# Kernel tuning notes

Measured on AMD Instinct MI355X. Metric: run time of the kernel, lower is better.

The kernel has to match this reference:

```python
import jax, jax.numpy as jnp
import numpy as np

N, F, M, B = 100000, 256, 10, 32768
DECAY = 0.9


def setup_inputs() -> dict:
    key = jax.random.key(0)
    ks = jax.random.split(key, 16)
    s = 1.0 / np.sqrt(F)
    # forward args
    node_indices = jax.random.permutation(ks[0], N)[:B]  # unique indices
    node_features = jax.random.normal(ks[1], (B, F), jnp.float32)
    # per-node state
    hidden_states = jax.random.normal(ks[2], (N, F), jnp.float32) * 0.1
    cell_states = jax.random.normal(ks[3], (N, F), jnp.float32) * 0.1
    temporal_memory = jax.random.normal(ks[4], (N, M, F), jnp.float32) * 0.1
    memory_ptr = jax.random.randint(ks[5], (N,), 0, M)
    # LSTMCell params (gate order i, f, g, o as in torch)
    W_ih = jax.random.normal(ks[6], (4 * F, F), jnp.float32) * s
    W_hh = jax.random.normal(ks[7], (4 * F, F), jnp.float32) * s
    b_ih = jax.random.normal(ks[8], (4 * F,), jnp.float32) * s
    b_hh = jax.random.normal(ks[9], (4 * F,), jnp.float32) * s
    # attention read params
    Wq = jax.random.normal(ks[10], (F, F), jnp.float32) * s
    bq = jnp.zeros((F,), jnp.float32)
    Wk = jax.random.normal(ks[11], (F, F), jnp.float32) * s
    bk = jnp.zeros((F,), jnp.float32)
    Wv = jax.random.normal(ks[12], (F, F), jnp.float32) * s
    bv = jnp.zeros((F,), jnp.float32)
    return dict(node_indices=node_indices, node_features=node_features,
                hidden_states=hidden_states, cell_states=cell_states,
                temporal_memory=temporal_memory, memory_ptr=memory_ptr,
                W_ih=W_ih, W_hh=W_hh, b_ih=b_ih, b_hh=b_hh,
                Wq=Wq, bq=bq, Wk=Wk, bk=bk, Wv=Wv, bv=bv)


def reference(node_indices, node_features, hidden_states, cell_states,
              temporal_memory, memory_ptr, W_ih, W_hh, b_ih, b_hh,
              Wq, bq, Wk, bk, Wv, bv):
    idx = node_indices
    feat = node_features.shape[-1]
    # --- update_memory: LSTMCell on gathered per-node states ---
    h_prev = hidden_states[idx]              # (B, F)
    c_prev = cell_states[idx]                # (B, F)
    gates = node_features @ W_ih.T + b_ih + h_prev @ W_hh.T + b_hh
    i, f, g, o = jnp.split(gates, 4, axis=-1)
    c_new = jax.nn.sigmoid(f) * c_prev + jax.nn.sigmoid(i) * jnp.tanh(g)
    h_new = jax.nn.sigmoid(o) * jnp.tanh(c_new)
    # --- scatter into circular temporal memory + decay previous slot ---
    ptr = memory_ptr[idx]                    # (B,)
    tm = temporal_memory.at[idx, ptr].set(node_features)
    prev = ptr - 1                           # -1 wraps; decay only applied if ptr > 0
    old = tm[idx, prev]                      # (B, F)
    tm = tm.at[idx, prev].set(jnp.where((ptr > 0)[:, None], old * DECAY, old))
    # --- get_temporal_context: gather + tiny attention over M slots ---
    mem = tm[idx]                            # (B, M, F)
    q = h_new @ Wq.T + bq                    # (B, F)  hidden_states[idx] post-update == h_new
    k = mem @ Wk.T + bk                      # (B, M, F)
    v = mem @ Wv.T + bv                      # (B, M, F)
    scores = jnp.einsum('bf,bmf->bm', q, k) / jnp.sqrt(jnp.asarray(feat, q.dtype))
    w = jax.nn.softmax(scores, axis=-1)      # (B, M)
    context = jnp.einsum('bmf,bm->bf', v, w) # (B, F)
    return context
```

## Files before the change

kernel.cpp:

```cpp
#include <hip/hip_runtime.h>
#include <hip/hip_bf16.h>

constexpr int NB = 32768;
constexpr int NF = 256;
constexpr int NM = 10;
constexpr float DECAY = 0.9f;

using bf16x8 = __attribute__((ext_vector_type(8))) short;
using f32x4  = __attribute__((ext_vector_type(4))) float;

static __device__ __forceinline__ ushort f2bf(float x) {
    unsigned u = __float_as_uint(x);
    unsigned r = (u + 0x7fffu + ((u >> 16) & 1u)) >> 16;
    return (ushort)r;
}
static __device__ __forceinline__ float bf2f(ushort x) {
    return __uint_as_float(((unsigned)x) << 16);
}
static __device__ __forceinline__ float sigmoid_f(float x) {
    return 1.f / (1.f + __expf(-x));
}
static __device__ __forceinline__ float tanh_f(float x) {
    float e = __expf(2.f * x);
    return (e - 1.f) / (e + 1.f);
}
static __device__ __forceinline__ void gload16(const void* g, void* l) {
    __builtin_amdgcn_global_load_lds(
        (const __attribute__((address_space(1))) unsigned int*)g,
        (__attribute__((address_space(3))) unsigned int*)l, 16, 0, 0);
}
static __device__ __forceinline__ int swzb(int row, int byteInRow) {
    return (row * 512 + byteInRow) ^ ((row & 7) << 4);
}

constexpr int PB_ACAT = 16384;
constexpr int PB_WGI  = PB_ACAT + 1024;
constexpr int PB_WQKT = PB_WGI + 256;
constexpr int PB_WV   = PB_WQKT + 256;
constexpr int PB_TOT  = PB_WV + 1;

__global__ __launch_bounds__(256) void k_prep(
    const float* __restrict__ W_ih, const float* __restrict__ W_hh,
    const float* __restrict__ b_ih, const float* __restrict__ b_hh,
    const float* __restrict__ Wq, const float* __restrict__ bq,
    const float* __restrict__ Wk, const float* __restrict__ Wv,
    const float* __restrict__ nf, const float* __restrict__ hidden,
    const int* __restrict__ idx,
    ushort* __restrict__ Wg, float* __restrict__ bsum,
    ushort* __restrict__ WqkT, float* __restrict__ bqk,
    ushort* __restrict__ Wvb, ushort* __restrict__ Acat)
{
    const int blk = blockIdx.x, tid = threadIdx.x;
    if (blk < PB_ACAT) {
        int t = blk * 256 + tid;
        int row = t >> 7;
        int c4 = (t & 127) * 4;
        const float* src = (c4 < 256) ? (nf + (size_t)row * 256 + c4)
                                      : (hidden + (size_t)idx[row] * 256 + (c4 - 256));
        float4 v = *reinterpret_cast<const float4*>(src);
        ushort4 o;
        o.x = f2bf(v.x); o.y = f2bf(v.y); o.z = f2bf(v.z); o.w = f2bf(v.w);
        *reinterpret_cast<ushort4*>(Acat + (size_t)row * 512 + c4) = o;
    } else if (blk < PB_WGI) {
        int j = blk - PB_ACAT;
        for (int c = tid; c < 512; c += 256) {
            float v = (c < 256) ? W_ih[j * 256 + c] : W_hh[j * 256 + (c - 256)];
            Wg[j * 512 + c] = f2bf(v);
        }
        if (tid == 0) bsum[j] = b_ih[j] + b_hh[j];
    } else if (blk < PB_WQKT) {
        int i = blk - PB_WGI, a = tid;
        float s = 0.f;
#pragma unroll 8
        for (int j = 0; j < 256; ++j) s += Wq[j * 256 + a] * Wk[j * 256 + i];
        WqkT[i * 256 + a] = f2bf(s * 0.0625f);
    } else if (blk < PB_WV) {
        int t = (blk - PB_WQKT) * 256 + tid;
        Wvb[t] = f2bf(Wv[t]);
    } else {
        int i = tid;
        float s = 0.f;
#pragma unroll 8
        for (int j = 0; j < 256; ++j) s += bq[j] * Wk[j * 256 + i];
        bqk[i] = s * 0.0625f;
    }
}

__global__ __launch_bounds__(256) void k_gates2(
    const ushort* __restrict__ Acat, const ushort* __restrict__ Wg,
    const float* __restrict__ bsum, const int* __restrict__ idx,
    const float* __restrict__ cell, ushort* __restrict__ h_new)
{
    __shared__ ushort As[2][128 * 32];
    __shared__ ushort Bs[2][128 * 32];
    const int t = threadIdx.x;
    const int w = t >> 6, l = t & 63;
    const int wr = w >> 1, wc = w & 1;
    const int lr = l & 15, lk = l >> 4;

    const int flat = blockIdx.x;
    const int xc = flat & 7, grp = flat >> 3;
    const int by = grp & 7;
    const int bx = (grp >> 3) * 8 + xc;
    const int row0 = bx * 128;
    const int f0 = by * 32;

    f32x4 acc[4][4];
#pragma unroll
    for (int m = 0; m < 4; ++m)
#pragma unroll
        for (int g = 0; g < 4; ++g) acc[m][g] = f32x4{0.f, 0.f, 0.f, 0.f};

    const int srow = l >> 2;
    const int scol = (l & 3) * 8;
    const int u0 = w * 2, u1 = u0 + 1;
    const ushort* aS0 = Acat + (size_t)(row0 + u0 * 16 + srow) * 512 + scol;
    const ushort* aS1 = Acat + (size_t)(row0 + u1 * 16 + srow) * 512 + scol;
    const ushort* bS0 = Wg + (size_t)(w * 256 + f0 + srow) * 512 + scol;
    const ushort* bS1 = Wg + (size_t)(w * 256 + f0 + 16 + srow) * 512 + scol;
    ushort* aL0_0 = As[0] + u0 * 512; ushort* aL1_0 = As[0] + u1 * 512;
    ushort* aL0_1 = As[1] + u0 * 512; ushort* aL1_1 = As[1] + u1 * 512;
    ushort* bL0_0 = Bs[0] + (w * 32) * 32; ushort* bL1_0 = Bs[0] + (w * 32 + 16) * 32;
    ushort* bL0_1 = Bs[1] + (w * 32) * 32; ushort* bL1_1 = Bs[1] + (w * 32 + 16) * 32;

    for (int k0 = 0; k0 < 512; k0 += 64) {
        gload16(aS0 + k0,      aL0_0);
        gload16(aS1 + k0,      aL1_0);
        gload16(aS0 + k0 + 32, aL0_1);
        gload16(aS1 + k0 + 32, aL1_1);
        gload16(bS0 + k0,      bL0_0);
        gload16(bS1 + k0,      bL1_0);
        gload16(bS0 + k0 + 32, bL0_1);
        gload16(bS1 + k0 + 32, bL1_1);
        __syncthreads();
#pragma unroll
        for (int h = 0; h < 2; ++h) {
            bf16x8 af[4], bfr[4];
#pragma unroll
            for (int m = 0; m < 4; ++m)
                af[m] = *reinterpret_cast<const bf16x8*>(As[h] + (wr * 64 + m * 16 + lr) * 32 + lk * 8);
#pragma unroll
            for (int g = 0; g < 4; ++g)
                bfr[g] = *reinterpret_cast<const bf16x8*>(Bs[h] + (g * 32 + wc * 16 + lr) * 32 + lk * 8);
#pragma unroll
            for (int m = 0; m < 4; ++m)
#pragma unroll
                for (int g = 0; g < 4; ++g)
                    acc[m][g] = __builtin_amdgcn_mfma_f32_16x16x32_bf16(af[m], bfr[g], acc[m][g], 0, 0, 0);
        }
        __syncthreads();
    }

    const int f = f0 + wc * 16 + lr;
    float bs[4];
#pragma unroll
    for (int g = 0; g < 4; ++g) bs[g] = bsum[g * 256 + f];

    int nodev[4][4];
#pragma unroll
    for (int m = 0; m < 4; ++m)
#pragma unroll
        for (int r = 0; r < 4; ++r)
            nodev[m][r] = idx[row0 + wr * 64 + m * 16 + lk * 4 + r];

#pragma unroll
    for (int m = 0; m < 4; ++m) {
#pragma unroll
        for (int r = 0; r < 4; ++r) {
            float gi = acc[m][0][r] + bs[0];
            float gf = acc[m][1][r] + bs[1];
            float gg = acc[m][2][r] + bs[2];
            float go = acc[m][3][r] + bs[3];
            float cp = cell[(size_t)nodev[m][r] * 256 + f];
            float cn = sigmoid_f(gf) * cp + sigmoid_f(gi) * tanh_f(gg);
            float hn = sigmoid_f(go) * tanh_f(cn);
            int row = row0 + wr * 64 + m * 16 + lk * 4 + r;
            h_new[(size_t)row * 256 + f] = f2bf(hn);
        }
    }
}

__global__ __launch_bounds__(256) void k_attnout(
    const ushort* __restrict__ hnew, const ushort* __restrict__ WqkT,
    const float* __restrict__ bqk, const ushort* __restrict__ Wvb,
    const float* __restrict__ bv, const int* __restrict__ idx,
    const int* __restrict__ mptr, const float* __restrict__ tm,
    const float* __restrict__ nf, float* __restrict__ out)
{
    __shared__ ushort sC[16 * 256];
    char* sB = (char*)sC;
    const int t = threadIdx.x, w = t >> 6, l = t & 63;
    const int lr = l & 15, lk = l >> 4;
    const int row0 = blockIdx.x * 16;

    {
        f32x4 qa[4];
#pragma unroll
        for (int n = 0; n < 4; ++n) qa[n] = f32x4{0.f, 0.f, 0.f, 0.f};
        const ushort* ap = hnew + (size_t)(row0 + lr) * 256 + lk * 8;
        const ushort* bp[4];
#pragma unroll
        for (int n = 0; n < 4; ++n) bp[n] = WqkT + (size_t)(w * 64 + n * 16 + lr) * 256 + lk * 8;
#pragma unroll 2
        for (int k0 = 0; k0 < 256; k0 += 32) {
            bf16x8 a = *reinterpret_cast<const bf16x8*>(ap + k0);
            bf16x8 b[4];
#pragma unroll
            for (int n = 0; n < 4; ++n) b[n] = *reinterpret_cast<const bf16x8*>(bp[n] + k0);
#pragma unroll
            for (int n = 0; n < 4; ++n)
                qa[n] = __builtin_amdgcn_mfma_f32_16x16x32_bf16(a, b[n], qa[n], 0, 0, 0);
        }
#pragma unroll
        for (int n = 0; n < 4; ++n) {
            int colc = w * 64 + n * 16 + lr;
            float bbq = bqk[colc];
#pragma unroll
            for (int r = 0; r < 4; ++r) {
                int row = lk * 4 + r;
                *(ushort*)(sB + swzb(row, colc * 2)) = f2bf(qa[n][r] + bbq);
            }
        }
    }
    __syncthreads();

    {
        const int b0 = row0 + w * 4;
        int nodes[4], ptrs[4];
#pragma unroll
        for (int r = 0; r < 4; ++r) { nodes[r] = idx[b0 + r]; ptrs[r] = mptr[nodes[r]]; }

        for (int rr = 0; rr < 4; ++rr) {
            const int row = w * 4 + rr;
            const int b = b0 + rr;
            const int node = nodes[rr];
            const int ptr = ptrs[rr];
            ushort4 q4 = *(const ushort4*)(sB + swzb(row, l * 8));
            float q0 = bf2f(q4.x), q1 = bf2f(q4.y), q2 = bf2f(q4.z), q3 = bf2f(q4.w);
            const float* base = tm + (size_t)node * (NM * NF);
            const float* nfp = nf + (size_t)b * 256 + l * 4;

            float4 mem[NM];
            float sc[NM];
#pragma unroll
            for (int m = 0; m < NM; ++m) {
                float4 v = (m == ptr) ? *reinterpret_cast<const float4*>(nfp)
                                      : *reinterpret_cast<const float4*>(base + (size_t)m * 256 + l * 4);
                if (ptr > 0 && m == ptr - 1) { v.x *= DECAY; v.y *= DECAY; v.z *= DECAY; v.w *= DECAY; }
                mem[m] = v;
                sc[m] = q0 * v.x + q1 * v.y + q2 * v.z + q3 * v.w;
            }
#pragma unroll
            for (int m = 0; m < NM; ++m) {
                float s = sc[m];
#pragma unroll
                for (int d = 1; d < 64; d <<= 1) s += __shfl_xor(s, d, 64);
                sc[m] = s;
            }
            float mx = sc[0];
#pragma unroll
            for (int m = 1; m < NM; ++m) mx = fmaxf(mx, sc[m]);
            float e[NM], sum = 0.f;
#pragma unroll
            for (int m = 0; m < NM; ++m) { e[m] = __expf(sc[m] - mx); sum += e[m]; }
            float inv = 1.f / sum;
            float4 c = {0.f, 0.f, 0.f, 0.f};
#pragma unroll
            for (int m = 0; m < NM; ++m) {
                float wm = e[m] * inv;
                c.x += wm * mem[m].x; c.y += wm * mem[m].y; c.z += wm * mem[m].z; c.w += wm * mem[m].w;
            }
            ushort4 o;
            o.x = f2bf(c.x); o.y = f2bf(c.y); o.z = f2bf(c.z); o.w = f2bf(c.w);
            *(ushort4*)(sB + swzb(row, l * 8)) = o;
        }
    }
    __syncthreads();

    f32x4 acc[4];
#pragma unroll
    for (int n = 0; n < 4; ++n) acc[n] = f32x4{0.f, 0.f, 0.f, 0.f};
    const ushort* vptr[4];
#pragma unroll
    for (int n = 0; n < 4; ++n) vptr[n] = Wvb + (size_t)(w * 64 + n * 16 + lr) * 256 + lk * 8;

#pragma unroll 2
    for (int k = 0; k < 256; k += 32) {
        bf16x8 a = *reinterpret_cast<const bf16x8*>(sB + swzb(lr, (k + lk * 8) * 2));
        bf16x8 b[4];
#pragma unroll
        for (int n = 0; n < 4; ++n) b[n] = *reinterpret_cast<const bf16x8*>(vptr[n] + k);
#pragma unroll
        for (int n = 0; n < 4; ++n)
            acc[n] = __builtin_amdgcn_mfma_f32_16x16x32_bf16(a, b[n], acc[n], 0, 0, 0);
    }
#pragma unroll
    for (int n = 0; n < 4; ++n) {
        int colc = w * 64 + n * 16 + lr;
        float bbv = bv[colc];
#pragma unroll
        for (int r = 0; r < 4; ++r) {
            int row = lk * 4 + r;
            out[(size_t)(row0 + row) * 256 + colc] = acc[n][r] + bbv;
        }
    }
}

extern "C" void kernel_launch(void* const* d_in, const int* in_sizes, int n_in,
                              void* d_out, int out_size, void* d_ws, size_t ws_size,
                              hipStream_t stream) {
    const int*   node_indices = (const int*)  d_in[0];
    const float* node_feats   = (const float*)d_in[1];
    const float* hidden       = (const float*)d_in[2];
    const float* cell         = (const float*)d_in[3];
    const float* tmem         = (const float*)d_in[4];
    const int*   memory_ptr   = (const int*)  d_in[5];
    const float* W_ih         = (const float*)d_in[6];
    const float* W_hh         = (const float*)d_in[7];
    const float* b_ih         = (const float*)d_in[8];
    const float* b_hh         = (const float*)d_in[9];
    const float* Wq           = (const float*)d_in[10];
    const float* bq           = (const float*)d_in[11];
    const float* Wk           = (const float*)d_in[12];
    const float* Wv           = (const float*)d_in[14];
    const float* bv           = (const float*)d_in[15];

    char* ws = (char*)d_ws;
    size_t off = 0;
    auto alloc = [&](size_t bytes) { char* p = ws + off; off += (bytes + 255) & ~(size_t)255; return p; };

    ushort* Wg    = (ushort*)alloc((size_t)1024 * 512 * 2);
    ushort* WqkT  = (ushort*)alloc((size_t)256 * 256 * 2);
    ushort* Wvb   = (ushort*)alloc((size_t)256 * 256 * 2);
    float*  bqk   = (float*) alloc((size_t)256 * 4);
    float*  bsum  = (float*) alloc((size_t)1024 * 4);
    ushort* Acat  = (ushort*)alloc((size_t)NB * 512 * 2);
    ushort* hnew  = (ushort*)alloc((size_t)NB * 256 * 2);

    k_prep<<<PB_TOT, 256, 0, stream>>>(W_ih, W_hh, b_ih, b_hh, Wq, bq, Wk, Wv,
                                       node_feats, hidden, node_indices,
                                       Wg, bsum, WqkT, bqk, Wvb, Acat);
    k_gates2<<<2048, 256, 0, stream>>>(Acat, Wg, bsum, node_indices, cell, hnew);
    k_attnout<<<NB / 16, 256, 0, stream>>>(hnew, WqkT, bqk, Wvb, bv, node_indices,
                                           memory_ptr, tmem, node_feats, (float*)d_out);
}
```

Baseline: 207.7 us.

## Widen gates GEMM tile to 64 features per block with 8 waves

The LSTM gates GEMM block tile grows from 128 rows x 32 features (x4 gates) to 128 rows x 64 features, using 512 threads (8 waves) and 1024 blocks instead of 2048. Each A tile loaded into shared memory now serves twice as many output columns, which halves redundant global reads of the concatenated input. The load distribution is rebuilt so each wave issues six 16-row chunk copies. The trade-off is more LDS per block (48 KB) and fewer resident blocks, which may reduce occupancy and latency hiding.

```diff
diff --git a/kernel.cpp b/kernel.cpp
--- a/kernel.cpp
+++ b/kernel.cpp
@@ -86,24 +86,24 @@
     }
 }
 
-__global__ __launch_bounds__(256) void k_gates2(
+__global__ __launch_bounds__(512) void k_gates2(
     const ushort* __restrict__ Acat, const ushort* __restrict__ Wg,
     const float* __restrict__ bsum, const int* __restrict__ idx,
     const float* __restrict__ cell, ushort* __restrict__ h_new)
 {
     __shared__ ushort As[2][128 * 32];
-    __shared__ ushort Bs[2][128 * 32];
+    __shared__ ushort Bs[2][256 * 32];
     const int t = threadIdx.x;
     const int w = t >> 6, l = t & 63;
-    const int wr = w >> 1, wc = w & 1;
+    const int wr = w >> 2, wc = w & 3;
     const int lr = l & 15, lk = l >> 4;
 
     const int flat = blockIdx.x;
     const int xc = flat & 7, grp = flat >> 3;
-    const int by = grp & 7;
-    const int bx = (grp >> 3) * 8 + xc;
+    const int by = grp & 3;
+    const int bx = (grp >> 2) * 8 + xc;
     const int row0 = bx * 128;
-    const int f0 = by * 32;
+    const int f0 = by * 64;
 
     f32x4 acc[4][4];
 #pragma unroll
@@ -113,25 +113,26 @@
 
     const int srow = l >> 2;
     const int scol = (l & 3) * 8;
-    const int u0 = w * 2, u1 = u0 + 1;
-    const ushort* aS0 = Acat + (size_t)(row0 + u0 * 16 + srow) * 512 + scol;
-    const ushort* aS1 = Acat + (size_t)(row0 + u1 * 16 + srow) * 512 + scol;
-    const ushort* bS0 = Wg + (size_t)(w * 256 + f0 + srow) * 512 + scol;
-    const ushort* bS1 = Wg + (size_t)(w * 256 + f0 + 16 + srow) * 512 + scol;
-    ushort* aL0_0 = As[0] + u0 * 512; ushort* aL1_0 = As[0] + u1 * 512;
-    ushort* aL0_1 = As[1] + u0 * 512; ushort* aL1_1 = As[1] + u1 * 512;
-    ushort* bL0_0 = Bs[0] + (w * 32) * 32; ushort* bL1_0 = Bs[0] + (w * 32 + 16) * 32;
-    ushort* bL0_1 = Bs[1] + (w * 32) * 32; ushort* bL1_1 = Bs[1] + (w * 32 + 16) * 32;
+    const ushort* src[6];
+    ushort* dst[6];
+#pragma unroll
+    for (int j = 0; j < 6; ++j) {
+        int q = w * 6 + j;
+        int h = q / 24, c = q % 24;
+        if (c < 8) {
+            src[j] = Acat + (size_t)(row0 + c * 16 + srow) * 512 + h * 32 + scol;
+            dst[j] = As[h] + c * 512;
+        } else {
+            int cb = c - 8;
+            int g = cb >> 2, fi0 = (cb & 3) * 16;
+            src[j] = Wg + (size_t)(g * 256 + f0 + fi0 + srow) * 512 + h * 32 + scol;
+            dst[j] = Bs[h] + cb * 512;
+        }
+    }
 
     for (int k0 = 0; k0 < 512; k0 += 64) {
-        gload16(aS0 + k0,      aL0_0);
-        gload16(aS1 + k0,      aL1_0);
-        gload16(aS0 + k0 + 32, aL0_1);
-        gload16(aS1 + k0 + 32, aL1_1);
-        gload16(bS0 + k0,      bL0_0);
-        gload16(bS1 + k0,      bL1_0);
-        gload16(bS0 + k0 + 32, bL0_1);
-        gload16(bS1 + k0 + 32, bL1_1);
+#pragma unroll
+        for (int j = 0; j < 6; ++j) gload16(src[j] + k0, dst[j]);
         __syncthreads();
 #pragma unroll
         for (int h = 0; h < 2; ++h) {
@@ -141,7 +142,7 @@
                 af[m] = *reinterpret_cast<const bf16x8*>(As[h] + (wr * 64 + m * 16 + lr) * 32 + lk * 8);
 #pragma unroll
             for (int g = 0; g < 4; ++g)
-                bfr[g] = *reinterpret_cast<const bf16x8*>(Bs[h] + (g * 32 + wc * 16 + lr) * 32 + lk * 8);
+                bfr[g] = *reinterpret_cast<const bf16x8*>(Bs[h] + (g * 64 + wc * 16 + lr) * 32 + lk * 8);
 #pragma unroll
             for (int m = 0; m < 4; ++m)
 #pragma unroll
@@ -340,7 +341,7 @@
     k_prep<<<PB_TOT, 256, 0, stream>>>(W_ih, W_hh, b_ih, b_hh, Wq, bq, Wk, Wv,
                                        node_feats, hidden, node_indices,
                                        Wg, bsum, WqkT, bqk, Wvb, Acat);
-    k_gates2<<<2048, 256, 0, stream>>>(Acat, Wg, bsum, node_indices, cell, hnew);
+    k_gates2<<<1024, 512, 0, stream>>>(Acat, Wg, bsum, node_indices, cell, hnew);
     k_attnout<<<NB / 16, 256, 0, stream>>>(hnew, WqkT, bqk, Wvb, bv, node_indices,
                                            memory_ptr, tmem, node_feats, (float*)d_out);
 }
```

Measured after the change: 200.7 us. 3.4% less time.
